# Optimization experiments

Hardware: AMD Instinct MI355X
Metric: run time of the kernel (lower is better)

## Reference

```python
import jax, jax.numpy as jnp
import numpy as np
import math

S = 64.0
M = 0.5
COS_M = math.cos(M)
SIN_M = math.sin(M)
TH = math.cos(math.pi - M)
MM = math.sin(math.pi - M) * M
NUM_CLASSES = 100000
EMB_DIM = 512
BATCH = 512
EPS_CLAMP = 1e-07


def setup_inputs() -> dict:
    key = jax.random.key(0)
    k1, k2, k3 = jax.random.split(key, 3)
    embeddings = jax.random.normal(k1, (BATCH, EMB_DIM), dtype=jnp.float32)
    weight = jax.random.normal(k2, (NUM_CLASSES, EMB_DIM), dtype=jnp.float32)
    labels = jax.random.randint(k3, (BATCH,), 0, NUM_CLASSES, dtype=jnp.int64)
    return {"embeddings": embeddings, "weight": weight, "labels": labels}


def _l2_normalize(x, axis=-1, eps=1e-12):
    # matches F.normalize(p=2): divide by max(norm, eps)
    norm = jnp.sqrt(jnp.sum(x * x, axis=axis, keepdims=True))
    return x / jnp.maximum(norm, eps)


def reference(embeddings, weight, labels):
    e = _l2_normalize(embeddings, axis=1)          # [B, D]
    w = _l2_normalize(weight, axis=1)              # [C, D]
    cosine = jnp.clip(e @ w.T, -1.0 + EPS_CLAMP, 1.0 - EPS_CLAMP)  # [B, C]
    sine = jnp.sqrt(1.0 - cosine * cosine)
    phi = cosine * COS_M - sine * SIN_M
    phi = jnp.where(cosine > TH, phi, cosine - MM)
    one_hot = jax.nn.one_hot(labels, NUM_CLASSES, dtype=cosine.dtype)
    logits = (one_hot * phi + (1.0 - one_hot) * cosine) * S
    # cross-entropy with mean reduction
    logp = jax.nn.log_softmax(logits, axis=-1)
    nll = -jnp.take_along_axis(logp, labels[:, None], axis=1)[:, 0]
    return jnp.mean(nll)
```

## Files before the change

kernel.cpp:

```cpp
#include <hip/hip_runtime.h>
#include <math.h>

#define BATCH 512
#define DIM 512
#define NCLS 100000
#define NB_TILES 782
#define S_SCALE 64.0f
#define COS_M 0.8775825618903728f
#define SIN_M 0.479425538604203f
#define TH_C (-0.8775825618903728f)
#define MM_C 0.2397127693021015f
#define CLIP_LO (-1.0f + 1e-7f)
#define CLIP_HI (1.0f - 1e-7f)

typedef __attribute__((ext_vector_type(8))) short bf16x8;
typedef __attribute__((ext_vector_type(4))) float f32x4;

__device__ __forceinline__ unsigned int f2bf(float x) {
    union { float f; unsigned int u; } v;
    v.f = x;
    return (v.u + 0x7fffu + ((v.u >> 16) & 1u)) >> 16;
}
__device__ __forceinline__ unsigned int pack2(float lo, float hi) {
    return f2bf(lo) | (f2bf(hi) << 16);
}

__global__ void k_norm_e(const float* __restrict__ e, short* __restrict__ ebf,
                         float* __restrict__ sumexpz) {
    int row = blockIdx.x;
    int tid = threadIdx.x;
    const float4* p = (const float4*)(e + (size_t)row * DIM);
    float4 v = p[tid];
    float ss = v.x * v.x + v.y * v.y + v.z * v.z + v.w * v.w;
    for (int m = 1; m < 64; m <<= 1) ss += __shfl_xor(ss, m, 64);
    __shared__ float wss[2];
    if ((tid & 63) == 0) wss[tid >> 6] = ss;
    __syncthreads();
    float inv = 1.0f / fmaxf(sqrtf(wss[0] + wss[1]), 1e-12f);
    ushort4 o;
    o.x = (unsigned short)f2bf(v.x * inv);
    o.y = (unsigned short)f2bf(v.y * inv);
    o.z = (unsigned short)f2bf(v.z * inv);
    o.w = (unsigned short)f2bf(v.w * inv);
    ((ushort4*)(ebf + (size_t)row * DIM))[tid] = o;
    if (tid == 0) sumexpz[row] = 0.0f;
}

__global__ __launch_bounds__(256, 2) void k_gemm(
    const short* __restrict__ ebf, const float* __restrict__ wgt,
    const int* __restrict__ labels, float* __restrict__ sumexp,
    float* __restrict__ phiS) {
    __shared__ __align__(16) short As[128 * 32];
    __shared__ __align__(16) short Bs[128 * 32];
    __shared__ int sLbl[128];
    __shared__ float sWn[128];

    int bx = blockIdx.x;
    int nb = (bx >> 5) * 8 + (bx & 7);
    if (nb >= NB_TILES) return;
    int mb = (bx >> 3) & 3;
    int n0 = nb * 128;

    int tid = threadIdx.x;
    int lane = tid & 63;
    int wv = tid >> 6;
    int wm = wv >> 1, wn = wv & 1;
    int quad = lane >> 4, l16 = lane & 15;

    if (tid < 128) sLbl[tid] = labels[mb * 128 + tid];

    int ar = tid >> 2;
    const short* gA = ebf + (size_t)(mb * 128 + ar) * DIM + (tid & 3) * 8;
    int akey = ((tid >> 2) ^ (tid >> 4)) & 3;
    int aw0 = ar * 32 + ((tid & 3) ^ akey) * 8;

    int br = tid >> 3;
    int gBo[4];
#pragma unroll
    for (int i = 0; i < 4; ++i) {
        int wr = n0 + 32 * i + br;
        if (wr > NCLS - 1) wr = NCLS - 1;
        gBo[i] = wr * DIM + (tid & 7) * 4;
    }
    int bkey = ((tid >> 3) ^ (tid >> 5)) & 3;
    int bw0 = br * 32 + (((tid & 7) >> 1) ^ bkey) * 8 + (tid & 1) * 4;

    f32x4 acc[4][4];
#pragma unroll
    for (int i = 0; i < 4; ++i)
#pragma unroll
        for (int j = 0; j < 4; ++j) acc[i][j] = (f32x4){0.f, 0.f, 0.f, 0.f};
    float ssq[4] = {0.f, 0.f, 0.f, 0.f};

    int go = (quad ^ ((l16 ^ (l16 >> 2)) & 3)) * 8;
    int arowb = (wm * 64 + l16) * 32 + go;
    int browb = (wn * 64 + l16) * 32 + go;

    int4 ra0 = *(const int4*)(gA);
    int4 ra1 = *(const int4*)(gA + 64 * DIM);
    float4 rb0 = *(const float4*)(wgt + gBo[0]);
    float4 rb1 = *(const float4*)(wgt + gBo[1]);
    float4 rb2 = *(const float4*)(wgt + gBo[2]);
    float4 rb3 = *(const float4*)(wgt + gBo[3]);

#pragma unroll 1
    for (int kc = 0; kc < 16; ++kc) {
        *(int4*)&As[aw0] = ra0;
        *(int4*)&As[64 * 32 + aw0] = ra1;
        {
            uint2 p;
            ssq[0] += rb0.x * rb0.x + rb0.y * rb0.y + rb0.z * rb0.z + rb0.w * rb0.w;
            p.x = pack2(rb0.x, rb0.y); p.y = pack2(rb0.z, rb0.w);
            *(uint2*)&Bs[bw0] = p;
            ssq[1] += rb1.x * rb1.x + rb1.y * rb1.y + rb1.z * rb1.z + rb1.w * rb1.w;
            p.x = pack2(rb1.x, rb1.y); p.y = pack2(rb1.z, rb1.w);
            *(uint2*)&Bs[1024 + bw0] = p;
            ssq[2] += rb2.x * rb2.x + rb2.y * rb2.y + rb2.z * rb2.z + rb2.w * rb2.w;
            p.x = pack2(rb2.x, rb2.y); p.y = pack2(rb2.z, rb2.w);
            *(uint2*)&Bs[2048 + bw0] = p;
            ssq[3] += rb3.x * rb3.x + rb3.y * rb3.y + rb3.z * rb3.z + rb3.w * rb3.w;
            p.x = pack2(rb3.x, rb3.y); p.y = pack2(rb3.z, rb3.w);
            *(uint2*)&Bs[3072 + bw0] = p;
        }
        if (kc < 15) {
            int ko = (kc + 1) * 32;
            ra0 = *(const int4*)(gA + ko);
            ra1 = *(const int4*)(gA + 64 * DIM + ko);
            rb0 = *(const float4*)(wgt + gBo[0] + ko);
            rb1 = *(const float4*)(wgt + gBo[1] + ko);
            rb2 = *(const float4*)(wgt + gBo[2] + ko);
            rb3 = *(const float4*)(wgt + gBo[3] + ko);
        }
        asm volatile("s_waitcnt lgkmcnt(0)\n\ts_barrier" ::: "memory");
        {
            bf16x8 af[4], bfr[4];
#pragma unroll
            for (int t = 0; t < 4; ++t)
                af[t] = *(const bf16x8*)&As[arowb + t * 16 * 32];
#pragma unroll
            for (int t = 0; t < 4; ++t)
                bfr[t] = *(const bf16x8*)&Bs[browb + t * 16 * 32];
#pragma unroll
            for (int tm = 0; tm < 4; ++tm)
#pragma unroll
                for (int tn = 0; tn < 4; ++tn)
                    acc[tm][tn] = __builtin_amdgcn_mfma_f32_16x16x32_bf16(
                        af[tm], bfr[tn], acc[tm][tn], 0, 0, 0);
        }
        asm volatile("s_barrier" ::: "memory");
    }

#pragma unroll
    for (int i = 0; i < 4; ++i) {
        float s = ssq[i];
        s += __shfl_xor(s, 1, 64);
        s += __shfl_xor(s, 2, 64);
        s += __shfl_xor(s, 4, 64);
        if ((lane & 7) == 0)
            sWn[32 * i + br] = 1.0f / fmaxf(sqrtf(s), 1e-12f);
    }
    asm volatile("s_waitcnt lgkmcnt(0)\n\ts_barrier" ::: "memory");

    float wscale[4];
#pragma unroll
    for (int tn = 0; tn < 4; ++tn) wscale[tn] = sWn[wn * 64 + tn * 16 + l16];

    float rowsum[16];
#pragma unroll
    for (int i = 0; i < 16; ++i) rowsum[i] = 0.0f;

#pragma unroll
    for (int tm = 0; tm < 4; ++tm) {
#pragma unroll
        for (int r = 0; r < 4; ++r) {
            int m_local = wm * 64 + tm * 16 + quad * 4 + r;
            int lbl = sLbl[m_local];
            float rs = 0.0f;
#pragma unroll
            for (int tn = 0; tn < 4; ++tn) {
                float c = acc[tm][tn][r] * wscale[tn];
                c = fminf(fmaxf(c, CLIP_LO), CLIP_HI);
                int col = n0 + wn * 64 + tn * 16 + l16;
                float t = c;
                if (col == lbl) {
                    float sn = sqrtf(fmaxf(1.0f - c * c, 0.0f));
                    float ph = c * COS_M - sn * SIN_M;
                    ph = (c > TH_C) ? ph : (c - MM_C);
                    t = ph;
                    phiS[mb * 128 + m_local] = S_SCALE * ph;
                }
                float ex = (col < NCLS) ? __expf(S_SCALE * t - 64.0f) : 0.0f;
                rs += ex;
            }
            rowsum[tm * 4 + r] = rs;
        }
    }
#pragma unroll
    for (int idx = 0; idx < 16; ++idx) {
        float v = rowsum[idx];
        v += __shfl_xor(v, 1, 64);
        v += __shfl_xor(v, 2, 64);
        v += __shfl_xor(v, 4, 64);
        v += __shfl_xor(v, 8, 64);
        if (l16 == idx) {
            int tm = idx >> 2, r = idx & 3;
            int m_local = wm * 64 + tm * 16 + quad * 4 + r;
            atomicAdd(&sumexp[mb * 128 + m_local], v);
        }
    }
}

__global__ void k_final(const float* __restrict__ sumexp,
                        const float* __restrict__ phiS,
                        float* __restrict__ out) {
    int tid = threadIdx.x;
    float nll = 64.0f + logf(sumexp[tid]) - phiS[tid];
    for (int m = 1; m < 64; m <<= 1) nll += __shfl_xor(nll, m, 64);
    __shared__ float ws[8];
    if ((tid & 63) == 0) ws[tid >> 6] = nll;
    __syncthreads();
    if (tid == 0) {
        float s = 0.0f;
        for (int j = 0; j < 8; ++j) s += ws[j];
        out[0] = s / (float)BATCH;
    }
}

extern "C" void kernel_launch(void* const* d_in, const int* in_sizes, int n_in,
                              void* d_out, int out_size, void* d_ws,
                              size_t ws_size, hipStream_t stream) {
    const float* emb = (const float*)d_in[0];
    const float* wgt = (const float*)d_in[1];
    const int* lbl = (const int*)d_in[2];

    char* ws = (char*)d_ws;
    short* ebf = (short*)ws;
    float* sumexp = (float*)(ws + 524288);
    float* phiS = (float*)(ws + 526336);

    k_norm_e<<<dim3(BATCH), dim3(128), 0, stream>>>(emb, ebf, sumexp);
    k_gemm<<<dim3(3136), dim3(256), 0, stream>>>(ebf, wgt, lbl, sumexp, phiS);
    k_final<<<dim3(1), dim3(512), 0, stream>>>(sumexp, phiS, (float*)d_out);
}
```

Before: 424.7 us.

## Cover the full batch per block so each weight tile is loaded once

```diff
diff --git a/kernel.cpp b/kernel.cpp
--- a/kernel.cpp
+++ b/kernel.cpp
@@ -46,67 +46,67 @@
     if (tid == 0) sumexpz[row] = 0.0f;
 }
 
-__global__ __launch_bounds__(256, 2) void k_gemm(
+__global__ __launch_bounds__(512, 2) void k_gemm(
     const short* __restrict__ ebf, const float* __restrict__ wgt,
     const int* __restrict__ labels, float* __restrict__ sumexp,
     float* __restrict__ phiS) {
-    __shared__ __align__(16) short As[128 * 32];
+    __shared__ __align__(16) short As[512 * 32];
     __shared__ __align__(16) short Bs[128 * 32];
-    __shared__ int sLbl[128];
+    __shared__ int sLbl[512];
     __shared__ float sWn[128];
 
-    int bx = blockIdx.x;
-    int nb = (bx >> 5) * 8 + (bx & 7);
-    if (nb >= NB_TILES) return;
-    int mb = (bx >> 3) & 3;
+    int nb = blockIdx.x;
     int n0 = nb * 128;
 
     int tid = threadIdx.x;
     int lane = tid & 63;
     int wv = tid >> 6;
-    int wm = wv >> 1, wn = wv & 1;
+    int wm = wv >> 1;
+    int wn = wv & 1;
     int quad = lane >> 4, l16 = lane & 15;
 
-    if (tid < 128) sLbl[tid] = labels[mb * 128 + tid];
+    sLbl[tid] = labels[tid];
 
     int ar = tid >> 2;
-    const short* gA = ebf + (size_t)(mb * 128 + ar) * DIM + (tid & 3) * 8;
-    int akey = ((tid >> 2) ^ (tid >> 4)) & 3;
+    const short* gA = ebf + (size_t)ar * DIM + (tid & 3) * 8;
+    int akey = (ar ^ (ar >> 2)) & 3;
     int aw0 = ar * 32 + ((tid & 3) ^ akey) * 8;
 
     int br = tid >> 3;
-    int gBo[4];
-#pragma unroll
-    for (int i = 0; i < 4; ++i) {
-        int wr = n0 + 32 * i + br;
+    int gBo[2];
+#pragma unroll
+    for (int i = 0; i < 2; ++i) {
+        int wr = n0 + 64 * i + br;
         if (wr > NCLS - 1) wr = NCLS - 1;
         gBo[i] = wr * DIM + (tid & 7) * 4;
     }
-    int bkey = ((tid >> 3) ^ (tid >> 5)) & 3;
+    int bkey = (br ^ (br >> 2)) & 3;
     int bw0 = br * 32 + (((tid & 7) >> 1) ^ bkey) * 8 + (tid & 1) * 4;
 
-    f32x4 acc[4][4];
-#pragma unroll
-    for (int i = 0; i < 4; ++i)
+    f32x4 acc[8][4];
+#pragma unroll
+    for (int i = 0; i < 8; ++i)
 #pragma unroll
         for (int j = 0; j < 4; ++j) acc[i][j] = (f32x4){0.f, 0.f, 0.f, 0.f};
-    float ssq[4] = {0.f, 0.f, 0.f, 0.f};
+    float ssq[2] = {0.f, 0.f};
 
     int go = (quad ^ ((l16 ^ (l16 >> 2)) & 3)) * 8;
-    int arowb = (wm * 64 + l16) * 32 + go;
+    int arowb = (wm * 128 + l16) * 32 + go;
     int browb = (wn * 64 + l16) * 32 + go;
 
     int4 ra0 = *(const int4*)(gA);
-    int4 ra1 = *(const int4*)(gA + 64 * DIM);
+    int4 ra1 = *(const int4*)(gA + 128 * DIM);
+    int4 ra2 = *(const int4*)(gA + 256 * DIM);
+    int4 ra3 = *(const int4*)(gA + 384 * DIM);
     float4 rb0 = *(const float4*)(wgt + gBo[0]);
     float4 rb1 = *(const float4*)(wgt + gBo[1]);
-    float4 rb2 = *(const float4*)(wgt + gBo[2]);
-    float4 rb3 = *(const float4*)(wgt + gBo[3]);
 
 #pragma unroll 1
     for (int kc = 0; kc < 16; ++kc) {
         *(int4*)&As[aw0] = ra0;
-        *(int4*)&As[64 * 32 + aw0] = ra1;
+        *(int4*)&As[128 * 32 + aw0] = ra1;
+        *(int4*)&As[256 * 32 + aw0] = ra2;
+        *(int4*)&As[384 * 32 + aw0] = ra3;
         {
             uint2 p;
             ssq[0] += rb0.x * rb0.x + rb0.y * rb0.y + rb0.z * rb0.z + rb0.w * rb0.w;
@@ -114,50 +114,43 @@
             *(uint2*)&Bs[bw0] = p;
             ssq[1] += rb1.x * rb1.x + rb1.y * rb1.y + rb1.z * rb1.z + rb1.w * rb1.w;
             p.x = pack2(rb1.x, rb1.y); p.y = pack2(rb1.z, rb1.w);
-            *(uint2*)&Bs[1024 + bw0] = p;
-            ssq[2] += rb2.x * rb2.x + rb2.y * rb2.y + rb2.z * rb2.z + rb2.w * rb2.w;
-            p.x = pack2(rb2.x, rb2.y); p.y = pack2(rb2.z, rb2.w);
             *(uint2*)&Bs[2048 + bw0] = p;
-            ssq[3] += rb3.x * rb3.x + rb3.y * rb3.y + rb3.z * rb3.z + rb3.w * rb3.w;
-            p.x = pack2(rb3.x, rb3.y); p.y = pack2(rb3.z, rb3.w);
-            *(uint2*)&Bs[3072 + bw0] = p;
         }
         if (kc < 15) {
             int ko = (kc + 1) * 32;
             ra0 = *(const int4*)(gA + ko);
-            ra1 = *(const int4*)(gA + 64 * DIM + ko);
+            ra1 = *(const int4*)(gA + 128 * DIM + ko);
+            ra2 = *(const int4*)(gA + 256 * DIM + ko);
+            ra3 = *(const int4*)(gA + 384 * DIM + ko);
             rb0 = *(const float4*)(wgt + gBo[0] + ko);
             rb1 = *(const float4*)(wgt + gBo[1] + ko);
-            rb2 = *(const float4*)(wgt + gBo[2] + ko);
-            rb3 = *(const float4*)(wgt + gBo[3] + ko);
         }
         asm volatile("s_waitcnt lgkmcnt(0)\n\ts_barrier" ::: "memory");
         {
-            bf16x8 af[4], bfr[4];
-#pragma unroll
-            for (int t = 0; t < 4; ++t)
-                af[t] = *(const bf16x8*)&As[arowb + t * 16 * 32];
-#pragma unroll
-            for (int t = 0; t < 4; ++t)
-                bfr[t] = *(const bf16x8*)&Bs[browb + t * 16 * 32];
-#pragma unroll
-            for (int tm = 0; tm < 4; ++tm)
+            bf16x8 bfr[4];
+#pragma unroll
+            for (int tn = 0; tn < 4; ++tn)
+                bfr[tn] = *(const bf16x8*)&Bs[browb + tn * 16 * 32];
+#pragma unroll
+            for (int tm = 0; tm < 8; ++tm) {
+                bf16x8 af = *(const bf16x8*)&As[arowb + tm * 16 * 32];
 #pragma unroll
                 for (int tn = 0; tn < 4; ++tn)
                     acc[tm][tn] = __builtin_amdgcn_mfma_f32_16x16x32_bf16(
-                        af[tm], bfr[tn], acc[tm][tn], 0, 0, 0);
+                        af, bfr[tn], acc[tm][tn], 0, 0, 0);
+            }
         }
         asm volatile("s_barrier" ::: "memory");
     }
 
 #pragma unroll
-    for (int i = 0; i < 4; ++i) {
+    for (int i = 0; i < 2; ++i) {
         float s = ssq[i];
         s += __shfl_xor(s, 1, 64);
         s += __shfl_xor(s, 2, 64);
         s += __shfl_xor(s, 4, 64);
         if ((lane & 7) == 0)
-            sWn[32 * i + br] = 1.0f / fmaxf(sqrtf(s), 1e-12f);
+            sWn[64 * i + br] = 1.0f / fmaxf(sqrtf(s), 1e-12f);
     }
     asm volatile("s_waitcnt lgkmcnt(0)\n\ts_barrier" ::: "memory");
 
@@ -165,15 +158,11 @@
 #pragma unroll
     for (int tn = 0; tn < 4; ++tn) wscale[tn] = sWn[wn * 64 + tn * 16 + l16];
 
-    float rowsum[16];
-#pragma unroll
-    for (int i = 0; i < 16; ++i) rowsum[i] = 0.0f;
-
-#pragma unroll
-    for (int tm = 0; tm < 4; ++tm) {
+#pragma unroll
+    for (int tm = 0; tm < 8; ++tm) {
 #pragma unroll
         for (int r = 0; r < 4; ++r) {
-            int m_local = wm * 64 + tm * 16 + quad * 4 + r;
+            int m_local = wm * 128 + tm * 16 + quad * 4 + r;
             int lbl = sLbl[m_local];
             float rs = 0.0f;
 #pragma unroll
@@ -187,25 +176,15 @@
                     float ph = c * COS_M - sn * SIN_M;
                     ph = (c > TH_C) ? ph : (c - MM_C);
                     t = ph;
-                    phiS[mb * 128 + m_local] = S_SCALE * ph;
+                    phiS[m_local] = S_SCALE * ph;
                 }
-                float ex = (col < NCLS) ? __expf(S_SCALE * t - 64.0f) : 0.0f;
-                rs += ex;
+                rs += (col < NCLS) ? __expf(S_SCALE * t - 64.0f) : 0.0f;
             }
-            rowsum[tm * 4 + r] = rs;
-        }
-    }
-#pragma unroll
-    for (int idx = 0; idx < 16; ++idx) {
-        float v = rowsum[idx];
-        v += __shfl_xor(v, 1, 64);
-        v += __shfl_xor(v, 2, 64);
-        v += __shfl_xor(v, 4, 64);
-        v += __shfl_xor(v, 8, 64);
-        if (l16 == idx) {
-            int tm = idx >> 2, r = idx & 3;
-            int m_local = wm * 64 + tm * 16 + quad * 4 + r;
-            atomicAdd(&sumexp[mb * 128 + m_local], v);
+            rs += __shfl_xor(rs, 1, 64);
+            rs += __shfl_xor(rs, 2, 64);
+            rs += __shfl_xor(rs, 4, 64);
+            rs += __shfl_xor(rs, 8, 64);
+            if (l16 == ((tm * 4 + r) & 15)) atomicAdd(&sumexp[m_local], rs);
         }
     }
 }
@@ -239,6 +218,6 @@
     float* phiS = (float*)(ws + 526336);
 
     k_norm_e<<<dim3(BATCH), dim3(128), 0, stream>>>(emb, ebf, sumexp);
-    k_gemm<<<dim3(3136), dim3(256), 0, stream>>>(ebf, wgt, lbl, sumexp, phiS);
+    k_gemm<<<dim3(NB_TILES), dim3(512), 0, stream>>>(ebf, wgt, lbl, sumexp, phiS);
     k_final<<<dim3(1), dim3(512), 0, stream>>>(sumexp, phiS, (float*)d_out);
 }
```

After: 492.3 us. 15.9% more time.

## Pre-convert weights to bf16 and stream tiles via direct-to-LDS triple buffering

Applied to the files above, without the earlier changes.

```diff
diff --git a/kernel.cpp b/kernel.cpp
--- a/kernel.cpp
+++ b/kernel.cpp
@@ -23,6 +23,12 @@
 }
 __device__ __forceinline__ unsigned int pack2(float lo, float hi) {
     return f2bf(lo) | (f2bf(hi) << 16);
+}
+
+__device__ __forceinline__ void gld_lds16(const void* g, void* l) {
+    __builtin_amdgcn_global_load_lds(
+        (const __attribute__((address_space(1))) void*)g,
+        (__attribute__((address_space(3))) void*)l, 16, 0, 0);
 }
 
 __global__ void k_norm_e(const float* __restrict__ e, short* __restrict__ ebf,
@@ -46,7 +52,167 @@
     if (tid == 0) sumexpz[row] = 0.0f;
 }
 
-__global__ __launch_bounds__(256, 2) void k_gemm(
+__global__ void k_wconv(const float* __restrict__ w, short* __restrict__ wbf,
+                        float* __restrict__ wnorm) {
+    int tid = threadIdx.x;
+    int row = blockIdx.x * 32 + (tid >> 3);
+    int j = tid & 7;
+    const float* src = w + (size_t)row * DIM + j * 4;
+    short* dst = wbf + (size_t)row * DIM + j * 4;
+    float ssq = 0.f;
+#pragma unroll
+    for (int k = 0; k < 16; ++k) {
+        float4 v = *(const float4*)(src + k * 32);
+        ssq += v.x * v.x + v.y * v.y + v.z * v.z + v.w * v.w;
+        uint2 p;
+        p.x = pack2(v.x, v.y);
+        p.y = pack2(v.z, v.w);
+        *(uint2*)(dst + k * 32) = p;
+    }
+    ssq += __shfl_xor(ssq, 1, 64);
+    ssq += __shfl_xor(ssq, 2, 64);
+    ssq += __shfl_xor(ssq, 4, 64);
+    if (j == 0) wnorm[row] = 1.0f / fmaxf(sqrtf(ssq), 1e-12f);
+}
+
+__global__ __launch_bounds__(256, 3) void k_gemm2(
+    const short* __restrict__ ebf, const short* __restrict__ wbf,
+    const float* __restrict__ wnorm, const int* __restrict__ labels,
+    float* __restrict__ sumexp, float* __restrict__ phiS) {
+    __shared__ __align__(16) short As[3][4096];
+    __shared__ __align__(16) short Bs[3][4096];
+    __shared__ int sLbl[128];
+
+    int bx = blockIdx.x;
+    int nb = (bx >> 5) * 8 + (bx & 7);
+    if (nb >= NB_TILES) return;
+    int mb = (bx >> 3) & 3;
+    int n0 = nb * 128;
+
+    int tid = threadIdx.x;
+    int lane = tid & 63;
+    int wv = tid >> 6;
+    int wm = wv >> 1, wn = wv & 1;
+    int quad = lane >> 4, l16 = lane & 15;
+
+    if (tid < 128) sLbl[tid] = labels[mb * 128 + tid];
+
+    int g = (lane & 3) ^ (((lane >> 2) ^ (lane >> 4)) & 3);
+    int r0 = wv * 16 + (lane >> 2);
+    int r1 = 64 + r0;
+    const char* gA0 = (const char*)ebf + (size_t)(mb * 128 + r0) * (DIM * 2) + g * 16;
+    const char* gA1 = (const char*)ebf + (size_t)(mb * 128 + r1) * (DIM * 2) + g * 16;
+    int wr0 = n0 + r0; if (wr0 > NCLS - 1) wr0 = NCLS - 1;
+    int wr1 = n0 + r1; if (wr1 > NCLS - 1) wr1 = NCLS - 1;
+    const char* gB0 = (const char*)wbf + (size_t)wr0 * (DIM * 2) + g * 16;
+    const char* gB1 = (const char*)wbf + (size_t)wr1 * (DIM * 2) + g * 16;
+    int ldsw = wv * 1024;
+
+#define STAGE(BUF, KC)                                                    \
+    do {                                                                  \
+        int kb_ = (KC) * 64;                                              \
+        gld_lds16(gA0 + kb_, (char*)&As[BUF][0] + ldsw);                  \
+        gld_lds16(gA1 + kb_, (char*)&As[BUF][0] + 4096 + ldsw);           \
+        gld_lds16(gB0 + kb_, (char*)&Bs[BUF][0] + ldsw);                  \
+        gld_lds16(gB1 + kb_, (char*)&Bs[BUF][0] + 4096 + ldsw);           \
+    } while (0)
+
+    f32x4 acc[4][4];
+#pragma unroll
+    for (int i = 0; i < 4; ++i)
+#pragma unroll
+        for (int j = 0; j < 4; ++j) acc[i][j] = (f32x4){0.f, 0.f, 0.f, 0.f};
+
+    int go = (quad ^ ((l16 ^ (l16 >> 2)) & 3)) * 8;
+    int arowb = (wm * 64 + l16) * 32 + go;
+    int browb = (wn * 64 + l16) * 32 + go;
+
+    STAGE(0, 0);
+    STAGE(1, 1);
+    asm volatile("s_waitcnt vmcnt(4)\n\ts_barrier" ::: "memory");
+
+#pragma unroll
+    for (int kc = 0; kc < 16; ++kc) {
+        int cur = kc % 3;
+        if (kc + 2 < 16) STAGE((kc + 2) % 3, kc + 2);
+        {
+            bf16x8 af[4], bfr[4];
+#pragma unroll
+            for (int t = 0; t < 4; ++t)
+                af[t] = *(const bf16x8*)&As[cur][arowb + t * 16 * 32];
+#pragma unroll
+            for (int t = 0; t < 4; ++t)
+                bfr[t] = *(const bf16x8*)&Bs[cur][browb + t * 16 * 32];
+#pragma unroll
+            for (int tm = 0; tm < 4; ++tm)
+#pragma unroll
+                for (int tn = 0; tn < 4; ++tn)
+                    acc[tm][tn] = __builtin_amdgcn_mfma_f32_16x16x32_bf16(
+                        af[tm], bfr[tn], acc[tm][tn], 0, 0, 0);
+        }
+        if (kc < 15) {
+            if (kc + 2 < 16)
+                asm volatile("s_waitcnt vmcnt(4)\n\ts_barrier" ::: "memory");
+            else
+                asm volatile("s_waitcnt vmcnt(0)\n\ts_barrier" ::: "memory");
+        }
+    }
+#undef STAGE
+
+    float wscale[4];
+#pragma unroll
+    for (int tn = 0; tn < 4; ++tn) {
+        int col = n0 + wn * 64 + tn * 16 + l16;
+        if (col > NCLS - 1) col = NCLS - 1;
+        wscale[tn] = wnorm[col];
+    }
+
+    float rowsum[16];
+#pragma unroll
+    for (int i = 0; i < 16; ++i) rowsum[i] = 0.0f;
+
+#pragma unroll
+    for (int tm = 0; tm < 4; ++tm) {
+#pragma unroll
+        for (int r = 0; r < 4; ++r) {
+            int m_local = wm * 64 + tm * 16 + quad * 4 + r;
+            int lbl = sLbl[m_local];
+            float rs = 0.0f;
+#pragma unroll
+            for (int tn = 0; tn < 4; ++tn) {
+                float c = acc[tm][tn][r] * wscale[tn];
+                c = fminf(fmaxf(c, CLIP_LO), CLIP_HI);
+                int col = n0 + wn * 64 + tn * 16 + l16;
+                float t = c;
+                if (col == lbl) {
+                    float sn = sqrtf(fmaxf(1.0f - c * c, 0.0f));
+                    float ph = c * COS_M - sn * SIN_M;
+                    ph = (c > TH_C) ? ph : (c - MM_C);
+                    t = ph;
+                    phiS[mb * 128 + m_local] = S_SCALE * ph;
+                }
+                float ex = (col < NCLS) ? __expf(S_SCALE * t - 64.0f) : 0.0f;
+                rs += ex;
+            }
+            rowsum[tm * 4 + r] = rs;
+        }
+    }
+#pragma unroll
+    for (int idx = 0; idx < 16; ++idx) {
+        float v = rowsum[idx];
+        v += __shfl_xor(v, 1, 64);
+        v += __shfl_xor(v, 2, 64);
+        v += __shfl_xor(v, 4, 64);
+        v += __shfl_xor(v, 8, 64);
+        if (l16 == idx) {
+            int tm = idx >> 2, r = idx & 3;
+            int m_local = wm * 64 + tm * 16 + quad * 4 + r;
+            atomicAdd(&sumexp[mb * 128 + m_local], v);
+        }
+    }
+}
+
+__global__ __launch_bounds__(256, 2) void k_gemm_fb(
     const short* __restrict__ ebf, const float* __restrict__ wgt,
     const int* __restrict__ labels, float* __restrict__ sumexp,
     float* __restrict__ phiS) {
@@ -237,8 +403,20 @@
     short* ebf = (short*)ws;
     float* sumexp = (float*)(ws + 524288);
     float* phiS = (float*)(ws + 526336);
-
-    k_norm_e<<<dim3(BATCH), dim3(128), 0, stream>>>(emb, ebf, sumexp);
-    k_gemm<<<dim3(3136), dim3(256), 0, stream>>>(ebf, wgt, lbl, sumexp, phiS);
+    float* wnorm = (float*)(ws + 528384);
+    short* wbf = (short*)(ws + 1048576);
+
+    const size_t NEED = 1048576ull + 102400000ull;
+
+    if (ws_size >= NEED) {
+        k_wconv<<<dim3(NCLS / 32), dim3(256), 0, stream>>>(wgt, wbf, wnorm);
+        k_norm_e<<<dim3(BATCH), dim3(128), 0, stream>>>(emb, ebf, sumexp);
+        k_gemm2<<<dim3(3136), dim3(256), 0, stream>>>(ebf, wbf, wnorm, lbl,
+                                                      sumexp, phiS);
+    } else {
+        k_norm_e<<<dim3(BATCH), dim3(128), 0, stream>>>(emb, ebf, sumexp);
+        k_gemm_fb<<<dim3(3136), dim3(256), 0, stream>>>(ebf, wgt, lbl, sumexp,
+                                                        phiS);
+    }
     k_final<<<dim3(1), dim3(512), 0, stream>>>(sumexp, phiS, (float*)d_out);
 }
```

Measured after the change: 490.2 us. +15.4%, slower.
